# Optimization experiments

Measured on AMD Instinct MI355X. Metric: run time of the kernel, lower is better.

Reference implementation:

```python
import jax, jax.numpy as jnp
import numpy as np

B, L, C, D = 8, 8192, 256, 256


def setup_inputs() -> dict:
    key = jax.random.key(0)
    ks = jax.random.split(key, 13)
    bound = 1.0 / np.sqrt(C)

    def W(k):
        return jax.random.uniform(k, (C, D), jnp.float32, -bound, bound)

    def b(k):
        return jax.random.uniform(k, (D,), jnp.float32, -bound, bound)

    return {
        "xs": jax.random.normal(ks[0], (B, L, C), jnp.float32),
        # forward-direction params
        "Wh1": W(ks[1]), "bh1": b(ks[2]),
        "Wz1": W(ks[3]), "bz1": b(ks[4]),
        "Ws1": W(ks[5]), "bs1": b(ks[6]),
        "h01": jnp.zeros((1, 1, D), jnp.float32),
        # backward-direction params
        "Wh_1": W(ks[7]), "bh_1": b(ks[8]),
        "Wz_1": W(ks[9]), "bz_1": b(ks[10]),
        "Ws_1": W(ks[11]), "bs_1": b(ks[12]),
        "h0_1": jnp.zeros((1, 1, D), jnp.float32),
    }


def _gru_scan(z, h_tilde, h0):
    """h[t] = z[t]*h_tilde[t] + (1-z[t])*h[t-1], h[-1]=h0. Parallel over time
    via associative scan on the affine maps h -> a*h + b."""
    a = 1.0 - z            # [B, L, D]
    b = z * h_tilde        # [B, L, D]

    def combine(c1, c2):
        a1, b1 = c1
        a2, b2 = c2
        return a1 * a2, a2 * b1 + b2

    A, Bc = jax.lax.associative_scan(combine, (a, b), axis=1)
    return Bc + A * h0     # broadcast h0 [1,1,D]


def reference(xs, Wh1, bh1, Wz1, bz1, Ws1, bs1, h01,
              Wh_1, bh_1, Wz_1, bz_1, Ws_1, bs_1, h0_1):
    sig = jax.nn.sigmoid
    # forward direction
    hf = _gru_scan(sig(xs @ Wz1 + bz1), xs @ Wh1 + bh1, h01) * sig(xs @ Ws1 + bs1)
    # backward direction: reverse time, scan, reverse back
    zr = sig(xs @ Wz_1 + bz_1)
    hr = xs @ Wh_1 + bh_1
    hb = _gru_scan(zr[:, ::-1], hr[:, ::-1], h0_1)[:, ::-1] * sig(xs @ Ws_1 + bs_1)
    return hf + hb
```

## Files before the change

kernel.cpp:

```cpp
#include <hip/hip_runtime.h>
#include <hip/hip_bf16.h>

typedef unsigned short u16;

#define BDIM 8
#define LDIM 8192
#define KDIM 256
#define DDIM 256
#define MTOT 65536
#define NDIM 1536
#define TCH  32
#define NCH  256


typedef float floatx4 __attribute__((ext_vector_type(4)));
typedef short bf16x8 __attribute__((ext_vector_type(8)));

__device__ __forceinline__ u16 f2bf(float f) {
  union { __hip_bfloat16 h; u16 u; } c;
  c.h = __float2bfloat16(f);
  return c.u;
}
__device__ __forceinline__ float bf2f(u16 u) {
  union { unsigned int i; float f; } c;
  c.i = ((unsigned int)u) << 16;
  return c.f;
}
__device__ __forceinline__ float sigmoidf_fast(float x) {
  return __builtin_amdgcn_rcpf(1.0f + __expf(-x));
}
__device__ __forceinline__ void gll16(const u16* g, u16* l) {
  __builtin_amdgcn_global_load_lds((const __attribute__((address_space(1))) void*)g,
                                   (__attribute__((address_space(3))) void*)l, 16, 0, 0);
}

__global__ void prep_weights(const float* __restrict__ Wh1, const float* __restrict__ Wz1,
                             const float* __restrict__ Ws1, const float* __restrict__ Wh_1,
                             const float* __restrict__ Wz_1, const float* __restrict__ Ws_1,
                             const float* __restrict__ bh1, const float* __restrict__ bz1,
                             const float* __restrict__ bs1, const float* __restrict__ bh_1,
                             const float* __restrict__ bz_1, const float* __restrict__ bs_1,
                             u16* __restrict__ WcatT, float* __restrict__ bcat) {
  const int n = blockIdx.x;
  const int k = threadIdx.x;
  const int dir = n / 768, r = n % 768;
  int d; const float* W; const float* bb;
  if (r < 512) {
    d = r >> 1;
    if (r & 1) { W = dir ? Wz_1 : Wz1; bb = dir ? bz_1 : bz1; }
    else       { W = dir ? Wh_1 : Wh1; bb = dir ? bh_1 : bh1; }
  } else {
    d = r - 512;
    W = dir ? Ws_1 : Ws1; bb = dir ? bs_1 : bs1;
  }
  WcatT[(size_t)n * KDIM + k] = f2bf(W[k * DDIM + d]);
  if (k == 0) bcat[n] = bb[d];
}

__global__ void convert_xs(const float* __restrict__ xs, u16* __restrict__ Abf) {
  size_t i = ((size_t)blockIdx.x * 256 + threadIdx.x) * 8;
  const float4* s = (const float4*)(xs + i);
  float4 f0 = s[0], f1 = s[1];
  union { u16 u[8]; uint4 v; } t;
  t.u[0] = f2bf(f0.x); t.u[1] = f2bf(f0.y); t.u[2] = f2bf(f0.z); t.u[3] = f2bf(f0.w);
  t.u[4] = f2bf(f1.x); t.u[5] = f2bf(f1.y); t.u[6] = f2bf(f1.z); t.u[7] = f2bf(f1.w);
  *(uint4*)(Abf + i) = t.v;
}

__global__ __launch_bounds__(256) void gemm_kernel(const u16* __restrict__ Abf,
                                                   const u16* __restrict__ WcatT,
                                                   const float* __restrict__ bcat,
                                                   u16* __restrict__ G) {
  __shared__ __align__(16) u16 As[8192];
  __shared__ __align__(16) u16 Bs[8192];
  const int tid = threadIdx.x;
  const int lane = tid & 63, wave = tid >> 6;
  const int wm = wave >> 1, wn = wave & 1;
  const int q = lane >> 4, r = lane & 15;

  const int xcd = blockIdx.x & 7;
  const int li  = blockIdx.x >> 3;
  const int mt  = xcd * 64 + li / 12;
  const int nt  = li % 12;
  const int m0 = mt * 128, n0 = nt * 128;

  const u16* gA[4]; const u16* gB[4]; u16* lA[4]; u16* lB[4];
#pragma unroll
  for (int j = 0; j < 4; j++) {
    const int bi = wave * 256 + j * 64 + lane;
    gA[j] = Abf   + (size_t)(m0 + (bi >> 3)) * KDIM + (bi & 7) * 8;
    gB[j] = WcatT + (size_t)(n0 + (bi >> 3)) * KDIM + (bi & 7) * 8;
    lA[j] = As + bi * 8;
    lB[j] = Bs + bi * 8;
  }

  floatx4 acc[4][4];
  floatx4 z4 = {0.f, 0.f, 0.f, 0.f};
#pragma unroll
  for (int i = 0; i < 4; i++)
#pragma unroll
    for (int j = 0; j < 4; j++) acc[i][j] = z4;

  for (int k0 = 0; k0 < KDIM; k0 += 64) {
#pragma unroll
    for (int j = 0; j < 4; j++) { gll16(gA[j] + k0, lA[j]); gll16(gB[j] + k0, lB[j]); }
    __syncthreads();
#pragma unroll
    for (int kk = 0; kk < 2; kk++) {
      bf16x8 af[4], bv[4];
#pragma unroll
      for (int i = 0; i < 4; i++)
        af[i] = *(const bf16x8*)(As + ((wm * 64 + i * 16 + r) * 8 + kk * 4 + q) * 8);
#pragma unroll
      for (int j = 0; j < 4; j++)
        bv[j] = *(const bf16x8*)(Bs + ((wn * 64 + j * 16 + r) * 8 + kk * 4 + q) * 8);
#pragma unroll
      for (int i = 0; i < 4; i++)
#pragma unroll
        for (int j = 0; j < 4; j++)
          acc[i][j] = __builtin_amdgcn_mfma_f32_16x16x32_bf16(af[i], bv[j], acc[i][j], 0, 0, 0);
    }
    __syncthreads();
  }

  float bvals[4];
#pragma unroll
  for (int j = 0; j < 4; j++) bvals[j] = bcat[n0 + wn * 64 + j * 16 + r];
#pragma unroll
  for (int i = 0; i < 4; i++) {
#pragma unroll
    for (int reg = 0; reg < 4; reg++) {
      size_t grow = (size_t)(m0 + wm * 64 + i * 16 + q * 4 + reg);
      u16* dst = G + grow * NDIM + n0 + wn * 64 + r;
#pragma unroll
      for (int j = 0; j < 4; j++)
        dst[j * 16] = f2bf(acc[i][j][reg] + bvals[j]);
    }
  }
}

__global__ __launch_bounds__(256) void scan_phaseA(const u16* __restrict__ G,
                                                   float* __restrict__ Acc,
                                                   float* __restrict__ Bcc) {
  const int slot = threadIdx.x >> 6, lane = threadIdx.x & 63;
  const int w = blockIdx.x * 4 + slot;
  const int u = w >> 1, half = w & 1;
  const int c = u & 255, b = (u >> 8) & 7, dir = u >> 11;
  const int d0 = half * 128 + lane * 2;
  const u16* p0 = G + (size_t)b * LDIM * NDIM + dir * 768 + d0 * 2;
  float h0 = 0.f, h1 = 0.f, P0 = 1.f, P1 = 1.f;
#pragma unroll 4
  for (int i = 0; i < TCH; ++i) {
    const int t = dir ? (c * TCH + (TCH - 1 - i)) : (c * TCH + i);
    uint2 hz = *(const uint2*)(p0 + (size_t)t * NDIM);
    const u16* q = (const u16*)&hz;
    float z0 = sigmoidf_fast(bf2f(q[1]));
    float z1 = sigmoidf_fast(bf2f(q[3]));
    float a0 = 1.f - z0, a1 = 1.f - z1;
    h0 = fmaf(a0, h0, z0 * bf2f(q[0]));
    h1 = fmaf(a1, h1, z1 * bf2f(q[2]));
    P0 *= a0; P1 *= a1;
  }
  float2 v;
  v.x = P0; v.y = P1;
  *(float2*)(Acc + (size_t)u * 256 + d0) = v;
  v.x = h0; v.y = h1;
  *(float2*)(Bcc + (size_t)u * 256 + d0) = v;
}

__global__ void scan_phaseB(const float* __restrict__ Acc, const float* __restrict__ Bcc,
                            const float* __restrict__ h01, const float* __restrict__ h0_1,
                            float* __restrict__ Pref) {
  const int d = threadIdx.x, b = blockIdx.x, dir = blockIdx.y;
  float h = dir ? h0_1[d] : h01[d];
  const size_t ubase = ((size_t)dir * BDIM + b) * NCH;
  if (dir == 0) {
    for (int c0 = 0; c0 < NCH; c0 += 8) {
      float a[8], bb[8];
#pragma unroll
      for (int j = 0; j < 8; ++j) {
        size_t idx = (ubase + c0 + j) * DDIM + d;
        a[j] = Acc[idx]; bb[j] = Bcc[idx];
      }
#pragma unroll
      for (int j = 0; j < 8; ++j) {
        Pref[(ubase + c0 + j) * DDIM + d] = h;
        h = fmaf(a[j], h, bb[j]);
      }
    }
  } else {
    for (int c0 = NCH - 1; c0 >= 0; c0 -= 8) {
      float a[8], bb[8];
#pragma unroll
      for (int j = 0; j < 8; ++j) {
        size_t idx = (ubase + c0 - j) * DDIM + d;
        a[j] = Acc[idx]; bb[j] = Bcc[idx];
      }
#pragma unroll
      for (int j = 0; j < 8; ++j) {
        Pref[(ubase + c0 - j) * DDIM + d] = h;
        h = fmaf(a[j], h, bb[j]);
      }
    }
  }
}

__global__ __launch_bounds__(256) void scan_phaseC(const u16* __restrict__ G,
                                                   const float* __restrict__ Pref,
                                                   float* __restrict__ out) {
  __shared__ float obuf[TCH * 256];
  const int c = blockIdx.x & 255, b = blockIdx.x >> 8;
  const int wave = threadIdx.x >> 6, lane = threadIdx.x & 63;
  const int dir = wave >> 1, half = wave & 1;
  const int d0 = half * 128 + lane * 2;
  const int u = dir * 2048 + b * 256 + c;
  float h0 = Pref[(size_t)u * 256 + d0];
  float h1 = Pref[(size_t)u * 256 + d0 + 1];
  const u16* ghz = G + (size_t)b * LDIM * NDIM + dir * 768 + d0 * 2;
  const u16* gs  = G + (size_t)b * LDIM * NDIM + dir * 768 + 512 + d0;

  if (dir == 1) {
#pragma unroll 4
    for (int i = 0; i < TCH; ++i) {
      const int tl = TCH - 1 - i;
      const int t = c * TCH + tl;
      uint2 hz = *(const uint2*)(ghz + (size_t)t * NDIM);
      unsigned int sv = *(const unsigned int*)(gs + (size_t)t * NDIM);
      const u16* q = (const u16*)&hz;
      const u16* sq = (const u16*)&sv;
      float z0 = sigmoidf_fast(bf2f(q[1]));
      float z1 = sigmoidf_fast(bf2f(q[3]));
      h0 = fmaf(1.f - z0, h0, z0 * bf2f(q[0]));
      h1 = fmaf(1.f - z1, h1, z1 * bf2f(q[2]));
      float2 o;
      o.x = h0 * sigmoidf_fast(bf2f(sq[0]));
      o.y = h1 * sigmoidf_fast(bf2f(sq[1]));
      *(float2*)(obuf + tl * 256 + d0) = o;
    }
  }
  __syncthreads();
  if (dir == 0) {
#pragma unroll 4
    for (int i = 0; i < TCH; ++i) {
      const int t = c * TCH + i;
      uint2 hz = *(const uint2*)(ghz + (size_t)t * NDIM);
      unsigned int sv = *(const unsigned int*)(gs + (size_t)t * NDIM);
      const u16* q = (const u16*)&hz;
      const u16* sq = (const u16*)&sv;
      float z0 = sigmoidf_fast(bf2f(q[1]));
      float z1 = sigmoidf_fast(bf2f(q[3]));
      h0 = fmaf(1.f - z0, h0, z0 * bf2f(q[0]));
      h1 = fmaf(1.f - z1, h1, z1 * bf2f(q[2]));
      float2 bb = *(const float2*)(obuf + i * 256 + d0);
      float2 o;
      o.x = fmaf(h0, sigmoidf_fast(bf2f(sq[0])), bb.x);
      o.y = fmaf(h1, sigmoidf_fast(bf2f(sq[1])), bb.y);
      *(float2*)(out + ((size_t)b * LDIM + t) * DDIM + d0) = o;
    }
  }
}

extern "C" void kernel_launch(void* const* d_in, const int* in_sizes, int n_in,
                              void* d_out, int out_size, void* d_ws, size_t ws_size,
                              hipStream_t stream) {
  const float* xs   = (const float*)d_in[0];
  const float* Wh1  = (const float*)d_in[1];
  const float* bh1  = (const float*)d_in[2];
  const float* Wz1  = (const float*)d_in[3];
  const float* bz1  = (const float*)d_in[4];
  const float* Ws1  = (const float*)d_in[5];
  const float* bs1  = (const float*)d_in[6];
  const float* h01  = (const float*)d_in[7];
  const float* Wh_1 = (const float*)d_in[8];
  const float* bh_1 = (const float*)d_in[9];
  const float* Wz_1 = (const float*)d_in[10];
  const float* bz_1 = (const float*)d_in[11];
  const float* Ws_1 = (const float*)d_in[12];
  const float* bs_1 = (const float*)d_in[13];
  const float* h0_1 = (const float*)d_in[14];
  float* out = (float*)d_out;

  char* ws = (char*)d_ws;
  u16* WcatT = (u16*)ws;   ws += (size_t)NDIM * KDIM * 2;
  float* bcat = (float*)ws; ws += (size_t)NDIM * 4;
  u16* Abf = (u16*)ws;     ws += (size_t)MTOT * KDIM * 2;
  u16* G = (u16*)ws;       ws += (size_t)MTOT * NDIM * 2;
  float* Acc  = (float*)Abf;
  float* Bcc  = Acc + (size_t)2 * BDIM * NCH * DDIM;
  float* Pref = Bcc + (size_t)2 * BDIM * NCH * DDIM;
  if ((size_t)(ws - (char*)d_ws) > ws_size) return;

  prep_weights<<<dim3(NDIM), dim3(KDIM), 0, stream>>>(
      Wh1, Wz1, Ws1, Wh_1, Wz_1, Ws_1, bh1, bz1, bs1, bh_1, bz_1, bs_1, WcatT, bcat);
  convert_xs<<<dim3(MTOT * KDIM / (256 * 8)), dim3(256), 0, stream>>>(xs, Abf);
  gemm_kernel<<<dim3(6144), dim3(256), 0, stream>>>(Abf, WcatT, bcat, G);
  scan_phaseA<<<dim3(2048), dim3(256), 0, stream>>>(G, Acc, Bcc);
  scan_phaseB<<<dim3(BDIM, 2), dim3(DDIM), 0, stream>>>(Acc, Bcc, h01, h0_1, Pref);
  scan_phaseC<<<dim3(2048), dim3(256), 0, stream>>>(G, Pref, out);
}
```

Baseline: 299.2 us.

## Swizzle GEMM LDS layout and run both scan directions concurrently in phase C

The GEMM tile loads now XOR-swizzle the 16-byte k-chunk index by row, so the MFMA fragment reads from LDS spread across banks instead of conflicting. Phase C grows to 512 threads with one channel per thread. The forward and backward directions now run their recurrences at the same time rather than one after the other, and the forward direction keeps its outputs in registers, then adds the backward buffer after a barrier. This adds register pressure from the 32-entry output array and narrows the per-thread global loads.

```diff
diff --git a/kernel.cpp b/kernel.cpp
--- a/kernel.cpp
+++ b/kernel.cpp
@@ -88,8 +88,10 @@
 #pragma unroll
   for (int j = 0; j < 4; j++) {
     const int bi = wave * 256 + j * 64 + lane;
-    gA[j] = Abf   + (size_t)(m0 + (bi >> 3)) * KDIM + (bi & 7) * 8;
-    gB[j] = WcatT + (size_t)(n0 + (bi >> 3)) * KDIM + (bi & 7) * 8;
+    const int row = bi >> 3;
+    const int kq = (bi & 7) ^ (row & 7);
+    gA[j] = Abf   + (size_t)(m0 + row) * KDIM + kq * 8;
+    gB[j] = WcatT + (size_t)(n0 + row) * KDIM + kq * 8;
     lA[j] = As + bi * 8;
     lB[j] = Bs + bi * 8;
   }
@@ -109,11 +111,15 @@
     for (int kk = 0; kk < 2; kk++) {
       bf16x8 af[4], bv[4];
 #pragma unroll
-      for (int i = 0; i < 4; i++)
-        af[i] = *(const bf16x8*)(As + ((wm * 64 + i * 16 + r) * 8 + kk * 4 + q) * 8);
-#pragma unroll
-      for (int j = 0; j < 4; j++)
-        bv[j] = *(const bf16x8*)(Bs + ((wn * 64 + j * 16 + r) * 8 + kk * 4 + q) * 8);
+      for (int i = 0; i < 4; i++) {
+        const int row = wm * 64 + i * 16 + r;
+        af[i] = *(const bf16x8*)(As + (row * 8 + ((kk * 4 + q) ^ (row & 7))) * 8);
+      }
+#pragma unroll
+      for (int j = 0; j < 4; j++) {
+        const int row = wn * 64 + j * 16 + r;
+        bv[j] = *(const bf16x8*)(Bs + (row * 8 + ((kk * 4 + q) ^ (row & 7))) * 8);
+      }
 #pragma unroll
       for (int i = 0; i < 4; i++)
 #pragma unroll
@@ -205,57 +211,47 @@
   }
 }
 
-__global__ __launch_bounds__(256) void scan_phaseC(const u16* __restrict__ G,
+__global__ __launch_bounds__(512) void scan_phaseC(const u16* __restrict__ G,
                                                    const float* __restrict__ Pref,
                                                    float* __restrict__ out) {
   __shared__ float obuf[TCH * 256];
   const int c = blockIdx.x & 255, b = blockIdx.x >> 8;
   const int wave = threadIdx.x >> 6, lane = threadIdx.x & 63;
-  const int dir = wave >> 1, half = wave & 1;
-  const int d0 = half * 128 + lane * 2;
+  const int dir = wave >> 2;
+  const int d0 = (wave & 3) * 64 + lane;
   const int u = dir * 2048 + b * 256 + c;
-  float h0 = Pref[(size_t)u * 256 + d0];
-  float h1 = Pref[(size_t)u * 256 + d0 + 1];
+  float h = Pref[(size_t)u * 256 + d0];
   const u16* ghz = G + (size_t)b * LDIM * NDIM + dir * 768 + d0 * 2;
   const u16* gs  = G + (size_t)b * LDIM * NDIM + dir * 768 + 512 + d0;
 
   if (dir == 1) {
-#pragma unroll 4
+#pragma unroll
     for (int i = 0; i < TCH; ++i) {
       const int tl = TCH - 1 - i;
       const int t = c * TCH + tl;
-      uint2 hz = *(const uint2*)(ghz + (size_t)t * NDIM);
-      unsigned int sv = *(const unsigned int*)(gs + (size_t)t * NDIM);
-      const u16* q = (const u16*)&hz;
-      const u16* sq = (const u16*)&sv;
-      float z0 = sigmoidf_fast(bf2f(q[1]));
-      float z1 = sigmoidf_fast(bf2f(q[3]));
-      h0 = fmaf(1.f - z0, h0, z0 * bf2f(q[0]));
-      h1 = fmaf(1.f - z1, h1, z1 * bf2f(q[2]));
-      float2 o;
-      o.x = h0 * sigmoidf_fast(bf2f(sq[0]));
-      o.y = h1 * sigmoidf_fast(bf2f(sq[1]));
-      *(float2*)(obuf + tl * 256 + d0) = o;
-    }
-  }
-  __syncthreads();
-  if (dir == 0) {
-#pragma unroll 4
+      unsigned int hz = *(const unsigned int*)(ghz + (size_t)t * NDIM);
+      u16 sv = gs[(size_t)t * NDIM];
+      float z = sigmoidf_fast(bf2f((u16)(hz >> 16)));
+      h = fmaf(1.f - z, h, z * bf2f((u16)(hz & 0xffff)));
+      obuf[tl * 256 + d0] = h * sigmoidf_fast(bf2f(sv));
+    }
+    __syncthreads();
+  } else {
+    float ov[TCH];
+#pragma unroll
     for (int i = 0; i < TCH; ++i) {
       const int t = c * TCH + i;
-      uint2 hz = *(const uint2*)(ghz + (size_t)t * NDIM);
-      unsigned int sv = *(const unsigned int*)(gs + (size_t)t * NDIM);
-      const u16* q = (const u16*)&hz;
-      const u16* sq = (const u16*)&sv;
-      float z0 = sigmoidf_fast(bf2f(q[1]));
-      float z1 = sigmoidf_fast(bf2f(q[3]));
-      h0 = fmaf(1.f - z0, h0, z0 * bf2f(q[0]));
-      h1 = fmaf(1.f - z1, h1, z1 * bf2f(q[2]));
-      float2 bb = *(const float2*)(obuf + i * 256 + d0);
-      float2 o;
-      o.x = fmaf(h0, sigmoidf_fast(bf2f(sq[0])), bb.x);
-      o.y = fmaf(h1, sigmoidf_fast(bf2f(sq[1])), bb.y);
-      *(float2*)(out + ((size_t)b * LDIM + t) * DDIM + d0) = o;
+      unsigned int hz = *(const unsigned int*)(ghz + (size_t)t * NDIM);
+      u16 sv = gs[(size_t)t * NDIM];
+      float z = sigmoidf_fast(bf2f((u16)(hz >> 16)));
+      h = fmaf(1.f - z, h, z * bf2f((u16)(hz & 0xffff)));
+      ov[i] = h * sigmoidf_fast(bf2f(sv));
+    }
+    __syncthreads();
+#pragma unroll
+    for (int i = 0; i < TCH; ++i) {
+      const int t = c * TCH + i;
+      out[((size_t)b * LDIM + t) * DDIM + d0] = ov[i] + obuf[i * 256 + d0];
     }
   }
 }
@@ -296,5 +292,5 @@
   gemm_kernel<<<dim3(6144), dim3(256), 0, stream>>>(Abf, WcatT, bcat, G);
   scan_phaseA<<<dim3(2048), dim3(256), 0, stream>>>(G, Acc, Bcc);
   scan_phaseB<<<dim3(BDIM, 2), dim3(DDIM), 0, stream>>>(Acc, Bcc, h01, h0_1, Pref);
-  scan_phaseC<<<dim3(2048), dim3(256), 0, stream>>>(G, Pref, out);
-}
+  scan_phaseC<<<dim3(2048), dim3(512), 0, stream>>>(G, Pref, out);
+}
```

New measurement: 293.4 us. Within noise of the previous version (-1.9%).
